# Optimization experiments

Measured on AMD Instinct MI355X. Metric: run time of the kernel, lower is better.

The kernel has to match this reference:

```python
import jax, jax.numpy as jnp
import numpy as np
from jax import lax

LOG2PI = float(np.log(2.0 * np.pi))
T, B, H, W, C = 64, 128, 64, 64, 3
A, LSTM_HID, LIN, CH, AH = 3, 512, 512, 256, 256
LSTM_IN = LIN + A + 1 + 1 + 1  # feats + last_action + last_reward + contact + time_till_end


def setup_inputs():
    key = jax.random.key(0)
    ks = jax.random.split(key, 32)

    def rn(i, shape, scale=1.0):
        return jax.random.normal(ks[i], shape, jnp.float32) * scale

    return {
        "x": rn(0, (T * B, H, W, C)),
        "done": jax.random.randint(ks[1], (T * B,), 0, 2, jnp.int32),
        "last_action": rn(2, (T * B, A)),
        "last_reward": rn(3, (T * B, 1)),
        "contact": jax.random.uniform(ks[4], (T * B, 1), jnp.float32),
        "time_till_end": jax.random.uniform(ks[5], (T * B, 1), jnp.float32),
        "action": rn(6, (T * B, A)),
        "h0": rn(7, (1, B, LSTM_HID)),
        "c0": rn(8, (1, B, LSTM_HID)),
        "conv1_w": rn(9, (8, 8, C, 32), 0.05), "conv1_b": jnp.zeros((32,), jnp.float32),
        "conv2_w": rn(10, (4, 4, 32, 64), 0.05), "conv2_b": jnp.zeros((64,), jnp.float32),
        "conv3_w": rn(11, (3, 3, 64, 64), 0.05), "conv3_b": jnp.zeros((64,), jnp.float32),
        "lin_w": rn(12, (1024, LIN), 0.03), "lin_b": jnp.zeros((LIN,), jnp.float32),
        "w_ih": rn(13, (4 * LSTM_HID, LSTM_IN), 0.02),
        "w_hh": rn(14, (4 * LSTM_HID, LSTM_HID), 0.02),
        "b_ih": jnp.zeros((4 * LSTM_HID,), jnp.float32),
        "b_hh": jnp.zeros((4 * LSTM_HID,), jnp.float32),
        "critic_w1": rn(15, (LSTM_HID, CH), 0.04), "critic_b1": jnp.zeros((CH,), jnp.float32),
        "critic_w2": rn(16, (CH, CH), 0.06), "critic_b2": jnp.zeros((CH,), jnp.float32),
        "critic_w3": rn(17, (CH, 1), 0.06), "critic_b3": jnp.zeros((1,), jnp.float32),
        "actor_w1": rn(18, (LSTM_HID, AH), 0.04), "actor_b1": jnp.zeros((AH,), jnp.float32),
        "actor_w2": rn(19, (AH, AH), 0.06), "actor_b2": jnp.zeros((AH,), jnp.float32),
        "actor_w3": rn(20, (AH, A), 0.01), "actor_b3": jnp.zeros((A,), jnp.float32),
        "actor_logstd": jnp.zeros((1, A), jnp.float32),
    }


def _conv(x, w, b, stride):
    y = lax.conv_general_dilated(x, w, (stride, stride), "VALID",
                                 dimension_numbers=("NHWC", "HWIO", "NHWC"))
    return jax.nn.relu(y + b)


def _mlp(v, w1, b1, w2, b2, w3, b3):
    v = jnp.tanh(v @ w1 + b1)
    v = jnp.tanh(v @ w2 + b2)
    return v @ w3 + b3


def reference(x, done, last_action, last_reward, contact, time_till_end, action, h0, c0,
              conv1_w, conv1_b, conv2_w, conv2_b, conv3_w, conv3_b, lin_w, lin_b,
              w_ih, w_hh, b_ih, b_hh,
              critic_w1, critic_b1, critic_w2, critic_b2, critic_w3, critic_b3,
              actor_w1, actor_b1, actor_w2, actor_b2, actor_w3, actor_b3, actor_logstd):
    batch = h0.shape[1]
    # CNN encoder (DQN-style)
    h = _conv(x, conv1_w, conv1_b, 4)            # [TB,15,15,32]
    h = _conv(h, conv2_w, conv2_b, 2)            # [TB,6,6,64]
    h = _conv(h, conv3_w, conv3_b, 1)            # [TB,4,4,64]
    h = h.reshape(h.shape[0], -1)                # [TB,1024]
    h = jax.nn.relu(h @ lin_w + lin_b)           # [TB,512]
    h = jnp.concatenate([h, last_action, last_reward, contact, time_till_end], axis=1)
    steps = h.shape[0] // batch
    xs = h.reshape(steps, batch, -1)             # [T,B,518]
    d = done.astype(h.dtype).reshape(steps, batch)

    def step(carry, inp):
        hs, cs = carry
        xt, dt = inp
        m = (1.0 - dt)[:, None]                  # reset state where done
        hs, cs = hs * m, cs * m
        z = xt @ w_ih.T + b_ih + hs @ w_hh.T + b_hh
        i, f, g, o = jnp.split(z, 4, axis=1)     # torch LSTM gate order i,f,g,o
        cs = jax.nn.sigmoid(f) * cs + jax.nn.sigmoid(i) * jnp.tanh(g)
        hs = jax.nn.sigmoid(o) * jnp.tanh(cs)
        return (hs, cs), hs

    (hN, cN), hid = lax.scan(step, (h0[0], c0[0]), (xs, d))
    hid = hid.reshape(steps * batch, -1)         # [TB,512]

    mean = _mlp(hid, actor_w1, actor_b1, actor_w2, actor_b2, actor_w3, actor_b3)
    logstd = jnp.broadcast_to(actor_logstd, mean.shape)
    inv_var = jnp.exp(-2.0 * logstd)
    logprob = (-0.5 * (action - mean) ** 2 * inv_var - logstd - 0.5 * LOG2PI).sum(axis=1)
    entropy = (0.5 + 0.5 * LOG2PI + logstd).sum(axis=1)
    value = _mlp(hid, critic_w1, critic_b1, critic_w2, critic_b2, critic_w3, critic_b3)
    return logprob, entropy, value, hN[None], cN[None]
```

## Files before the change

kernel.cpp:

```cpp
#include <hip/hip_runtime.h>
#include <hip/hip_bf16.h>
#include <cmath>

using bf16 = __hip_bfloat16;

#define DEV static __device__ __forceinline__

DEV float toF(float x) { return x; }
DEV float toF(bf16 x) { return __bfloat162float(x); }

DEV float loadF(const void* p, long i, int f32) {
    return f32 ? ((const float*)p)[i] : toF(((const bf16*)p)[i]);
}
DEV void storeOut(void* out, long i, float v, int f32) {
    if (f32) ((float*)out)[i] = v;
    else ((bf16*)out)[i] = __float2bfloat16(v);
}

__device__ __constant__ float kLOG2PI = 1.8378770664093453f;
DEV float sigf(float x) { return 1.0f / (1.0f + __expf(-x)); }

typedef __attribute__((ext_vector_type(4))) float fx4;
typedef __attribute__((ext_vector_type(8))) short s16x8;

static constexpr size_t OFF_WIHT  = 0;
static constexpr size_t OFF_WHHT  = 2121728;
static constexpr size_t OFF_BSUM  = 4218880;
static constexpr size_t OFF_LINB  = 4227072;
static constexpr size_t OFF_HB    = 4229120;
static constexpr size_t OFF_HT0   = 4233216;
static constexpr size_t OFF_HT1   = 4495360;
static constexpr size_t OFF_CT    = 4757504;
static constexpr size_t OFF_CW1   = 5019648;
static constexpr size_t OFF_CW2   = 5031936;
static constexpr size_t OFF_CW3   = 5097472;
static constexpr size_t OFF_CBIAS = 5171200;
static constexpr size_t OFF_ACT   = 5171840;
static constexpr size_t OFF_FB    = 5220992;
static constexpr size_t OFF_FLAG  = 5221024;
static constexpr size_t OFF_XIN   = 5221120;
static constexpr size_t OFF_C3H   = 13708032;
static constexpr size_t OFF_HID   = 22096640;
static constexpr size_t OFF_OUT2 = OFF_C3H;
static constexpr size_t OFF_OUT3 = OFF_C3H + 2359296;
static constexpr size_t OFF_LINW = OFF_C3H + 3407872;
static constexpr size_t OFF_OUT1 = OFF_HID;

__global__ void detect_k(const void* __restrict__ action, int* __restrict__ flag) {
    int lane = threadIdx.x;
    const unsigned short* p = (const unsigned short*)action;
    unsigned short v = p[lane];
    int e = (v >> 7) & 0xFF;
    bool bad = (e >= 0x8C);
    unsigned long long m = __ballot(bad);
    if (lane == 0) *flag = (m != 0ull) ? 1 : 0;
}

__global__ __launch_bounds__(256) void prep_k(
    const void* w_ih, const void* w_hh, const void* b_ih, const void* b_hh,
    const void* lin_b, const void* ab1, const void* ab2, const void* cb1, const void* cb2,
    const void* h0, const void* c0,
    const void* c1w, const void* c2w, const void* c3w,
    const void* c1b, const void* c2b, const void* c3b,
    const void* action, const void* ab3, const void* cb3, const void* logstd,
    bf16* __restrict__ wihT, bf16* __restrict__ whhT,
    float* __restrict__ bsum, float* __restrict__ linbf, float* __restrict__ hbias,
    float* __restrict__ hT0, float* __restrict__ cT,
    bf16* __restrict__ cw1, bf16* __restrict__ cw2, bf16* __restrict__ cw3,
    float* __restrict__ cbias, bf16* __restrict__ act, float* __restrict__ fb,
    const int* __restrict__ flagp,
    const void* lin_w, bf16* __restrict__ linwb)
{
    const int f = *flagp;
    long i = (long)blockIdx.x * 256 + threadIdx.x;
    if (i < 1060864) { long k = i >> 11, j = i & 2047;
        wihT[i] = __float2bfloat16(loadF(w_ih, j * 518 + k, f)); return; }
    i -= 1060864;
    if (i < 1048576) { long k = i >> 11, j = i & 2047;
        whhT[i] = __float2bfloat16(loadF(w_hh, j * 512 + k, f)); return; }
    i -= 1048576;
    if (i < 2048) { bsum[i] = loadF(b_ih, i, f) + loadF(b_hh, i, f); return; }
    i -= 2048;
    if (i < 512)  { linbf[i] = loadF(lin_b, i, f); return; }
    i -= 512;
    if (i < 1024) { int w = (int)(i >> 8), r = (int)(i & 255);
        const void* s = (w == 0) ? ab1 : (w == 1) ? ab2 : (w == 2) ? cb1 : cb2;
        hbias[i] = loadF(s, r, f); return; }
    i -= 1024;
    if (i < 65536) { long b = i & 127, k = i >> 7; hT0[i] = loadF(h0, b * 512 + k, f); return; }
    i -= 65536;
    if (i < 65536) { long b = i & 127, k = i >> 7; cT[i]  = loadF(c0, b * 512 + k, f); return; }
    i -= 65536;
    if (i < 6144)  { cw1[i] = __float2bfloat16(loadF(c1w, i, f)); return; }
    i -= 6144;
    if (i < 32768) { cw2[i] = __float2bfloat16(loadF(c2w, i, f)); return; }
    i -= 32768;
    if (i < 36864) { cw3[i] = __float2bfloat16(loadF(c3w, i, f)); return; }
    i -= 36864;
    if (i < 160) { float v = (i < 32) ? loadF(c1b, i, f)
                         : (i < 96) ? loadF(c2b, i - 32, f) : loadF(c3b, i - 96, f);
        cbias[i] = v; return; }
    i -= 160;
    if (i < 24576) { act[i] = __float2bfloat16(loadF(action, i, f)); return; }
    i -= 24576;
    if (i < 8) {
        float v = 0.f;
        if (i < 3) v = loadF(ab3, i, f);
        else if (i == 3) v = loadF(cb3, 0, f);
        else if (i < 7) v = loadF(logstd, i - 4, f);
        fb[i] = v; return;
    }
    i -= 8;
    if (i < 524288) { linwb[i] = __float2bfloat16(loadF(lin_w, i, f)); return; }
}

template <int BN, int MODE, int IC = 1, int KX = 1, int ST = 1, int IW = 1,
          int OW = 1, int OHW = 1>
__global__ __launch_bounds__(256) void mfma_gemm(
    const void* __restrict__ A, int lda,
    const bf16* __restrict__ B, int ldb,
    const float* __restrict__ bias,
    bf16* __restrict__ C, int ldc,
    int M, int N, int K, int ACT,
    const int* __restrict__ flagp, int imgBase)
{
    constexpr int BM = 128;
    constexpr int LSTR = 40;
    __shared__ __align__(16) bf16 As[BM * LSTR];
    __shared__ __align__(16) bf16 Bs[BN * LSTR];

    const int tid = threadIdx.x;
    const int lane = tid & 63, wave = tid >> 6;
    const int row0 = blockIdx.y * BM, col0 = blockIdx.x * BN;

    constexpr int NWN = (BN >= 64) ? 2 : 1;
    constexpr int WM = BM / (4 / NWN);
    constexpr int WN = BN / NWN;
    constexpr int FM = WM / 16, FN = WN / 16;
    const int wm = (wave / NWN) * WM;
    const int wn = (wave % NWN) * WN;

    fx4 acc[FM][FN] = {};

    const int am = tid >> 1;
    const int ak = (tid & 1) * 16;
    const int gm = row0 + am;
    int ibase = 0;
    if constexpr (MODE != 0) {
        int img = imgBase + gm / OHW;
        int s = gm % OHW;
        int oy = s / OW, ox = s % OW;
        ibase = (img * IW + oy * ST) * IW + ox * ST;
    }
    const int f32f = (MODE == 1) ? *flagp : 0;

    constexpr int KPT = BN / 8;
    const int nloc = tid & (BN - 1);
    const int kg0 = (tid / BN) * KPT;

    for (int k0 = 0; k0 < K; k0 += 32) {
        {
            bf16 tb[16];
            const int kk0 = k0 + ak;
            if constexpr (MODE == 0) {
                const unsigned short* Ab = (const unsigned short*)A + (long)gm * lda;
                if (kk0 + 16 <= K) {
                    const unsigned int* s4 = (const unsigned int*)(Ab + kk0);
                    unsigned int* d4 = (unsigned int*)tb;
                    #pragma unroll
                    for (int j = 0; j < 8; ++j) d4[j] = s4[j];
                } else {
                    unsigned short* bs = (unsigned short*)tb;
                    #pragma unroll
                    for (int j = 0; j < 16; ++j) {
                        int kg = kk0 + j;
                        bs[j] = (kg < K) ? Ab[kg] : (unsigned short)0;
                    }
                }
            } else {
                #pragma unroll
                for (int j = 0; j < 16; ++j) {
                    int kg = kk0 + j;
                    int ky = kg / (KX * IC);
                    int rem = kg - ky * (KX * IC);
                    int kx = rem / IC;
                    int ic = rem - kx * IC;
                    long idx = (long)(ibase + ky * IW + kx) * IC + ic;
                    if constexpr (MODE == 1)
                        tb[j] = __float2bfloat16(loadF(A, idx, f32f));
                    else
                        tb[j] = ((const bf16*)A)[idx];
                }
            }
            unsigned int* dst = (unsigned int*)(As + am * LSTR + ak);
            const unsigned int* src = (const unsigned int*)tb;
            #pragma unroll
            for (int j = 0; j < 8; ++j) dst[j] = src[j];
        }
        {
            bf16 tb[KPT];
            #pragma unroll
            for (int j = 0; j < KPT; ++j) {
                int kg = k0 + kg0 + j;
                unsigned short v = 0;
                if (kg < K) v = ((const unsigned short*)B)[(long)kg * ldb + col0 + nloc];
                ((unsigned short*)tb)[j] = v;
            }
            unsigned int* dst = (unsigned int*)(Bs + nloc * LSTR + kg0);
            const unsigned int* src = (const unsigned int*)tb;
            #pragma unroll
            for (int j = 0; j < KPT / 2; ++j) dst[j] = src[j];
        }
        __syncthreads();

        const int lr = lane & 15, lc = (lane >> 4) * 8;
        s16x8 af[FM], bfr[FN];
        #pragma unroll
        for (int i = 0; i < FM; ++i)
            af[i] = *(const s16x8*)(As + (wm + i * 16 + lr) * LSTR + lc);
        #pragma unroll
        for (int j = 0; j < FN; ++j)
            bfr[j] = *(const s16x8*)(Bs + (wn + j * 16 + lr) * LSTR + lc);
        #pragma unroll
        for (int i = 0; i < FM; ++i)
            #pragma unroll
            for (int j = 0; j < FN; ++j)
                acc[i][j] = __builtin_amdgcn_mfma_f32_16x16x32_bf16(
                    af[i], bfr[j], acc[i][j], 0, 0, 0);
        __syncthreads();
    }

    const int er = (lane >> 4) * 4, ec = lane & 15;
    #pragma unroll
    for (int i = 0; i < FM; ++i) {
        #pragma unroll
        for (int j = 0; j < FN; ++j) {
            const int cc = col0 + wn + j * 16 + ec;
            const float bv = bias[cc];
            #pragma unroll
            for (int r = 0; r < 4; ++r) {
                int rr = row0 + wm + i * 16 + er + r;
                float v = acc[i][j][r] + bv;
                if (ACT == 1) v = fmaxf(v, 0.f);
                C[(long)rr * ldc + cc] = __float2bfloat16(v);
            }
        }
    }
}

template <typename AT, typename OT, int BMODE, int ACT>
__global__ __launch_bounds__(256) void gemm_tiled(
    const AT* __restrict__ A, int lda,
    const void* __restrict__ B, int ldb,
    const float* __restrict__ bias,
    OT* __restrict__ C, int ldc,
    int M, int N, int K, const int* __restrict__ flagp)
{
    __shared__ float As[16][68];
    __shared__ float Bs[16][68];
    const int bF32 = (BMODE == 1) ? *flagp : 0;
    const int tid = threadIdx.x;
    const int tx = tid & 15, ty = tid >> 4;
    const int row0 = blockIdx.y * 64, col0 = blockIdx.x * 64;
    float acc[4][4] = {};
    for (int k0 = 0; k0 < K; k0 += 16) {
        #pragma unroll
        for (int i = 0; i < 4; ++i) {
            int idx = tid + i * 256;
            int m = idx >> 4, kk = idx & 15;
            int kg = k0 + kk;
            float v = 0.f;
            if (kg < K) v = toF(A[(size_t)(row0 + m) * lda + kg]);
            As[kk][m] = v;
        }
        #pragma unroll
        for (int i = 0; i < 4; ++i) {
            int idx = tid + i * 256;
            int n = idx & 63, kk = idx >> 6;
            int kg = k0 + kk;
            float v = 0.f;
            if (kg < K) {
                size_t bi = (size_t)kg * ldb + col0 + n;
                v = bF32 ? ((const float*)B)[bi] : toF(((const bf16*)B)[bi]);
            }
            Bs[kk][n] = v;
        }
        __syncthreads();
        #pragma unroll
        for (int kk = 0; kk < 16; ++kk) {
            float a[4], b[4];
            #pragma unroll
            for (int i = 0; i < 4; ++i) a[i] = As[kk][ty * 4 + i];
            #pragma unroll
            for (int j = 0; j < 4; ++j) b[j] = Bs[kk][tx * 4 + j];
            #pragma unroll
            for (int i = 0; i < 4; ++i)
                #pragma unroll
                for (int j = 0; j < 4; ++j)
                    acc[i][j] += a[i] * b[j];
        }
        __syncthreads();
    }
    #pragma unroll
    for (int i = 0; i < 4; ++i) {
        int r = row0 + ty * 4 + i;
        #pragma unroll
        for (int j = 0; j < 4; ++j) {
            int c = col0 + tx * 4 + j;
            float v = acc[i][j] + bias[c];
            if (ACT == 1) v = fmaxf(v, 0.f);
            if (ACT == 2) v = tanhf(v);
            if constexpr (sizeof(OT) == 2) C[(size_t)r * ldc + c] = __float2bfloat16(v);
            else                            C[(size_t)r * ldc + c] = v;
        }
    }
}

__global__ __launch_bounds__(256) void concat_k(
    const void* __restrict__ la, const void* __restrict__ lr,
    const void* __restrict__ ct, const void* __restrict__ tte,
    bf16* __restrict__ xin, const int* __restrict__ flagp)
{
    const int f = *flagp;
    int i = blockIdx.x * 256 + threadIdx.x;
    if (i >= 8192 * 6) return;
    int n = i / 6, e = i % 6;
    float v;
    if (e < 3) v = loadF(la, (long)n * 3 + e, f);
    else if (e == 3) v = loadF(lr, n, f);
    else if (e == 4) v = loadF(ct, n, f);
    else v = loadF(tte, n, f);
    xin[(size_t)n * 518 + 512 + e] = __float2bfloat16(v);
}

__global__ __launch_bounds__(256) void lstm_step(
    const bf16* __restrict__ zx,
    const bf16* __restrict__ whhT,
    const int* __restrict__ done,
    const float* __restrict__ hTin,
    float* __restrict__ hTout,
    float* __restrict__ cT,
    bf16* __restrict__ hid,
    int step)
{
    __shared__ float red[128][8];
    const int tid = threadIdx.x;
    const int b = tid & 127;
    const int kh = tid >> 7;
    const int j0 = blockIdx.x * 2;
    float acc[8] = {0.f, 0.f, 0.f, 0.f, 0.f, 0.f, 0.f, 0.f};
    const int kbeg = kh * 256;
    #pragma unroll 4
    for (int k = kbeg; k < kbeg + 256; ++k) {
        float hk = hTin[k * 128 + b];
        const bf16* wr = whhT + (size_t)k * 2048 + j0;
        #pragma unroll
        for (int g = 0; g < 4; ++g) {
            acc[g * 2 + 0] += hk * toF(wr[g * 512]);
            acc[g * 2 + 1] += hk * toF(wr[g * 512 + 1]);
        }
    }
    if (kh == 1) {
        #pragma unroll
        for (int q = 0; q < 8; ++q) red[b][q] = acc[q];
    }
    __syncthreads();
    if (kh == 0) {
        const int r = step * 128 + b;
        const long lr = (long)((step & 15) * 128 + b);
        const float m = done[r] ? 0.f : 1.f;
        #pragma unroll
        for (int jj = 0; jj < 2; ++jj) {
            int j = j0 + jj;
            float zi = toF(zx[lr * 2048 + 0 * 512 + j]) + m * (acc[0 + jj] + red[b][0 + jj]);
            float zf = toF(zx[lr * 2048 + 1 * 512 + j]) + m * (acc[2 + jj] + red[b][2 + jj]);
            float zg = toF(zx[lr * 2048 + 2 * 512 + j]) + m * (acc[4 + jj] + red[b][4 + jj]);
            float zo = toF(zx[lr * 2048 + 3 * 512 + j]) + m * (acc[6 + jj] + red[b][6 + jj]);
            float ig = sigf(zi), fg = sigf(zf), og = sigf(zo);
            float gg = tanhf(zg);
            float cold = cT[j * 128 + b] * m;
            float cn = fg * cold + ig * gg;
            float hn = og * tanhf(cn);
            cT[j * 128 + b] = cn;
            hTout[j * 128 + b] = hn;
            hid[(size_t)r * 512 + j] = __float2bfloat16(hn);
        }
    }
}

__global__ __launch_bounds__(256) void actor_final(
    const float* __restrict__ t2, const void* __restrict__ w3,
    const bf16* __restrict__ act, const float* __restrict__ fb,
    void* __restrict__ out, const int* __restrict__ flagp)
{
    const int f = *flagp;
    int lane = threadIdx.x & 63;
    int n = blockIdx.x * 4 + (threadIdx.x >> 6);
    const float* row = t2 + (size_t)n * 256;
    float s0 = 0.f, s1 = 0.f, s2 = 0.f;
    #pragma unroll
    for (int j = 0; j < 4; ++j) {
        int k = lane + j * 64;
        float v = row[k];
        s0 += v * loadF(w3, (long)k * 3 + 0, f);
        s1 += v * loadF(w3, (long)k * 3 + 1, f);
        s2 += v * loadF(w3, (long)k * 3 + 2, f);
    }
    #pragma unroll
    for (int off = 32; off > 0; off >>= 1) {
        s0 += __shfl_down(s0, off, 64);
        s1 += __shfl_down(s1, off, 64);
        s2 += __shfl_down(s2, off, 64);
    }
    if (lane == 0) {
        float mean[3] = {s0 + fb[0], s1 + fb[1], s2 + fb[2]};
        float lp = 0.f, ent = 0.f;
        #pragma unroll
        for (int a = 0; a < 3; ++a) {
            float ls = fb[4 + a];
            float iv = __expf(-2.f * ls);
            float d = toF(act[n * 3 + a]) - mean[a];
            lp += -0.5f * d * d * iv - ls - 0.5f * kLOG2PI;
            ent += 0.5f + 0.5f * kLOG2PI + ls;
        }
        storeOut(out, n, lp, f);
        storeOut(out, 8192 + n, ent, f);
    }
}

__global__ __launch_bounds__(256) void critic_final(
    const float* __restrict__ t2, const void* __restrict__ w3,
    const float* __restrict__ fb, void* __restrict__ out,
    const int* __restrict__ flagp)
{
    const int f = *flagp;
    int lane = threadIdx.x & 63;
    int n = blockIdx.x * 4 + (threadIdx.x >> 6);
    const float* row = t2 + (size_t)n * 256;
    float s = 0.f;
    #pragma unroll
    for (int j = 0; j < 4; ++j) {
        int k = lane + j * 64;
        s += row[k] * loadF(w3, k, f);
    }
    #pragma unroll
    for (int off = 32; off > 0; off >>= 1) s += __shfl_down(s, off, 64);
    if (lane == 0) storeOut(out, 16384 + n, s + fb[3], f);
}

__global__ __launch_bounds__(256) void state_out_k(
    const float* __restrict__ hT, const float* __restrict__ cT,
    void* __restrict__ out, const int* __restrict__ flagp)
{
    const int f = *flagp;
    int i = blockIdx.x * 256 + threadIdx.x;
    if (i >= 65536) return;
    int b = i >> 9, k = i & 511;
    storeOut(out, 24576 + i, hT[k * 128 + b], f);
    storeOut(out, 90112 + i, cT[k * 128 + b], f);
}

extern "C" void kernel_launch(void* const* d_in, const int* in_sizes, int n_in,
                              void* d_out, int out_size, void* d_ws, size_t ws_size,
                              hipStream_t stream)
{
    const void* x        = d_in[0];
    const int*  done     = (const int*)d_in[1];
    const void* last_act = d_in[2];
    const void* last_rew = d_in[3];
    const void* contact  = d_in[4];
    const void* tte      = d_in[5];
    const void* action   = d_in[6];
    const void* h0       = d_in[7];
    const void* c0       = d_in[8];
    const void* conv1_w  = d_in[9],  *conv1_b = d_in[10];
    const void* conv2_w  = d_in[11], *conv2_b = d_in[12];
    const void* conv3_w  = d_in[13], *conv3_b = d_in[14];
    const void* lin_w    = d_in[15], *lin_b   = d_in[16];
    const void* w_ih     = d_in[17], *w_hh    = d_in[18];
    const void* b_ih     = d_in[19], *b_hh    = d_in[20];
    const void* critic_w1 = d_in[21], *critic_b1 = d_in[22];
    const void* critic_w2 = d_in[23], *critic_b2 = d_in[24];
    const void* critic_w3 = d_in[25], *critic_b3 = d_in[26];
    const void* actor_w1  = d_in[27], *actor_b1  = d_in[28];
    const void* actor_w2  = d_in[29], *actor_b2  = d_in[30];
    const void* actor_w3  = d_in[31], *actor_b3  = d_in[32];
    const void* logstd    = d_in[33];

    char* ws = (char*)d_ws;
    bf16*  wihT  = (bf16*)(ws + OFF_WIHT);
    bf16*  whhT  = (bf16*)(ws + OFF_WHHT);
    float* bsum  = (float*)(ws + OFF_BSUM);
    float* linbf = (float*)(ws + OFF_LINB);
    float* hb    = (float*)(ws + OFF_HB);
    float* ab1f = hb + 0, *ab2f = hb + 256, *cb1f = hb + 512, *cb2f = hb + 768;
    float* hT0 = (float*)(ws + OFF_HT0);
    float* hT1 = (float*)(ws + OFF_HT1);
    float* cT  = (float*)(ws + OFF_CT);
    bf16*  cw1 = (bf16*)(ws + OFF_CW1);
    bf16*  cw2 = (bf16*)(ws + OFF_CW2);
    bf16*  cw3 = (bf16*)(ws + OFF_CW3);
    float* cbias = (float*)(ws + OFF_CBIAS);
    bf16*  act = (bf16*)(ws + OFF_ACT);
    float* fb  = (float*)(ws + OFF_FB);
    int*   flagp = (int*)(ws + OFF_FLAG);
    bf16*  xin = (bf16*)(ws + OFF_XIN);
    bf16*  zxb = (bf16*)(ws + OFF_C3H);
    bf16*  hid = (bf16*)(ws + OFF_HID);
    float* t1  = (float*)(ws + OFF_XIN);
    float* t2  = (float*)(ws + OFF_C3H);
    bf16*  out1  = (bf16*)(ws + OFF_OUT1);
    bf16*  out2  = (bf16*)(ws + OFF_OUT2);
    bf16*  out3  = (bf16*)(ws + OFF_OUT3);
    bf16*  linwb = (bf16*)(ws + OFF_LINW);

    detect_k<<<1, 64, 0, stream>>>(action, flagp);

    prep_k<<<11207, 256, 0, stream>>>(w_ih, w_hh, b_ih, b_hh, lin_b,
        actor_b1, actor_b2, critic_b1, critic_b2, h0, c0,
        conv1_w, conv2_w, conv3_w, conv1_b, conv2_b, conv3_b,
        action, actor_b3, critic_b3, logstd,
        wihT, whhT, bsum, linbf, hb, hT0, cT, cw1, cw2, cw3, cbias, act, fb, flagp,
        lin_w, linwb);

    for (int c = 0; c < 16; ++c) {
        const int ib = c * 512;
        mfma_gemm<32, 1, 3, 8, 4, 64, 15, 225><<<dim3(1, 900), 256, 0, stream>>>(
            x, 0, cw1, 32, cbias, out1, 32, 115200, 32, 192, 1, flagp, ib);
        mfma_gemm<64, 2, 32, 4, 2, 15, 6, 36><<<dim3(1, 144), 256, 0, stream>>>(
            out1, 0, cw2, 64, cbias + 32, out2, 64, 18432, 64, 512, 1, flagp, 0);
        mfma_gemm<64, 2, 64, 3, 1, 6, 4, 16><<<dim3(1, 64), 256, 0, stream>>>(
            out2, 0, cw3, 64, cbias + 96, out3, 64, 8192, 64, 576, 1, flagp, 0);
        mfma_gemm<64, 0><<<dim3(8, 4), 256, 0, stream>>>(
            out3, 1024, linwb, 512, linbf,
            xin + (size_t)ib * 518, 518, 512, 512, 1024, 1, flagp, 0);
    }
    concat_k<<<192, 256, 0, stream>>>(last_act, last_rew, contact, tte, xin, flagp);

    for (int chunk = 0; chunk < 4; ++chunk) {
        mfma_gemm<64, 0><<<dim3(32, 16), 256, 0, stream>>>(
            xin + (size_t)chunk * 2048 * 518, 518, wihT, 2048, bsum,
            zxb, 2048, 2048, 2048, 518, 0, flagp, 0);
        for (int t = chunk * 16; t < chunk * 16 + 16; ++t) {
            float* hin  = (t & 1) ? hT1 : hT0;
            float* hout = (t & 1) ? hT0 : hT1;
            lstm_step<<<256, 256, 0, stream>>>(zxb, whhT, done, hin, hout, cT, hid, t);
        }
    }

    gemm_tiled<bf16, float, 1, 2><<<dim3(4, 128), 256, 0, stream>>>(
        hid, 512, actor_w1, 256, ab1f, t1, 256, 8192, 256, 512, flagp);
    gemm_tiled<float, float, 1, 2><<<dim3(4, 128), 256, 0, stream>>>(
        t1, 256, actor_w2, 256, ab2f, t2, 256, 8192, 256, 256, flagp);
    actor_final<<<2048, 256, 0, stream>>>(t2, actor_w3, act, fb, d_out, flagp);

    gemm_tiled<bf16, float, 1, 2><<<dim3(4, 128), 256, 0, stream>>>(
        hid, 512, critic_w1, 256, cb1f, t1, 256, 8192, 256, 512, flagp);
    gemm_tiled<float, float, 1, 2><<<dim3(4, 128), 256, 0, stream>>>(
        t1, 256, critic_w2, 256, cb2f, t2, 256, 8192, 256, 256, flagp);
    critic_final<<<2048, 256, 0, stream>>>(t2, critic_w3, fb, d_out, flagp);

    state_out_k<<<256, 256, 0, stream>>>(hT0, cT, d_out, flagp);
}
```

Measured before the change: 6.183 ms.

## Fuse LSTM timesteps into persistent cooperative MFMA kernel and use MFMA for heads

```diff
diff --git a/kernel.cpp b/kernel.cpp
--- a/kernel.cpp
+++ b/kernel.cpp
@@ -1,6 +1,9 @@
 #include <hip/hip_runtime.h>
 #include <hip/hip_bf16.h>
+#include <hip/hip_cooperative_groups.h>
 #include <cmath>
+
+namespace cg = cooperative_groups;
 
 using bf16 = __hip_bfloat16;
 
@@ -65,7 +68,7 @@
     const void* action, const void* ab3, const void* cb3, const void* logstd,
     bf16* __restrict__ wihT, bf16* __restrict__ whhT,
     float* __restrict__ bsum, float* __restrict__ linbf, float* __restrict__ hbias,
-    float* __restrict__ hT0, float* __restrict__ cT,
+    bf16* __restrict__ h0b, float* __restrict__ cT,
     bf16* __restrict__ cw1, bf16* __restrict__ cw2, bf16* __restrict__ cw3,
     float* __restrict__ cbias, bf16* __restrict__ act, float* __restrict__ fb,
     const int* __restrict__ flagp,
@@ -87,7 +90,7 @@
         const void* s = (w == 0) ? ab1 : (w == 1) ? ab2 : (w == 2) ? cb1 : cb2;
         hbias[i] = loadF(s, r, f); return; }
     i -= 1024;
-    if (i < 65536) { long b = i & 127, k = i >> 7; hT0[i] = loadF(h0, b * 512 + k, f); return; }
+    if (i < 65536) { h0b[i] = __float2bfloat16(loadF(h0, i, f)); return; }
     i -= 65536;
     if (i < 65536) { long b = i & 127, k = i >> 7; cT[i]  = loadF(c0, b * 512 + k, f); return; }
     i -= 65536;
@@ -114,11 +117,11 @@
     if (i < 524288) { linwb[i] = __float2bfloat16(loadF(lin_w, i, f)); return; }
 }
 
-template <int BN, int MODE, int IC = 1, int KX = 1, int ST = 1, int IW = 1,
-          int OW = 1, int OHW = 1>
+template <int BN, int MODE, int BSRC = 0, int IC = 1, int KX = 1, int ST = 1,
+          int IW = 1, int OW = 1, int OHW = 1>
 __global__ __launch_bounds__(256) void mfma_gemm(
     const void* __restrict__ A, int lda,
-    const bf16* __restrict__ B, int ldb,
+    const void* __restrict__ B, int ldb,
     const float* __restrict__ bias,
     bf16* __restrict__ C, int ldc,
     int M, int N, int K, int ACT,
@@ -152,7 +155,7 @@
         int oy = s / OW, ox = s % OW;
         ibase = (img * IW + oy * ST) * IW + ox * ST;
     }
-    const int f32f = (MODE == 1) ? *flagp : 0;
+    const int f32f = (MODE == 1 || BSRC == 1) ? *flagp : 0;
 
     constexpr int KPT = BN / 8;
     const int nloc = tid & (BN - 1);
@@ -202,9 +205,15 @@
             #pragma unroll
             for (int j = 0; j < KPT; ++j) {
                 int kg = k0 + kg0 + j;
-                unsigned short v = 0;
-                if (kg < K) v = ((const unsigned short*)B)[(long)kg * ldb + col0 + nloc];
-                ((unsigned short*)tb)[j] = v;
+                if constexpr (BSRC == 1) {
+                    float v = 0.f;
+                    if (kg < K) v = loadF(B, (long)kg * ldb + col0 + nloc, f32f);
+                    tb[j] = __float2bfloat16(v);
+                } else {
+                    unsigned short v = 0;
+                    if (kg < K) v = ((const unsigned short*)B)[(long)kg * ldb + col0 + nloc];
+                    ((unsigned short*)tb)[j] = v;
+                }
             }
             unsigned int* dst = (unsigned int*)(Bs + nloc * LSTR + kg0);
             const unsigned int* src = (const unsigned int*)tb;
@@ -242,76 +251,9 @@
                 int rr = row0 + wm + i * 16 + er + r;
                 float v = acc[i][j][r] + bv;
                 if (ACT == 1) v = fmaxf(v, 0.f);
+                if (ACT == 2) v = tanhf(v);
                 C[(long)rr * ldc + cc] = __float2bfloat16(v);
             }
-        }
-    }
-}
-
-template <typename AT, typename OT, int BMODE, int ACT>
-__global__ __launch_bounds__(256) void gemm_tiled(
-    const AT* __restrict__ A, int lda,
-    const void* __restrict__ B, int ldb,
-    const float* __restrict__ bias,
-    OT* __restrict__ C, int ldc,
-    int M, int N, int K, const int* __restrict__ flagp)
-{
-    __shared__ float As[16][68];
-    __shared__ float Bs[16][68];
-    const int bF32 = (BMODE == 1) ? *flagp : 0;
-    const int tid = threadIdx.x;
-    const int tx = tid & 15, ty = tid >> 4;
-    const int row0 = blockIdx.y * 64, col0 = blockIdx.x * 64;
-    float acc[4][4] = {};
-    for (int k0 = 0; k0 < K; k0 += 16) {
-        #pragma unroll
-        for (int i = 0; i < 4; ++i) {
-            int idx = tid + i * 256;
-            int m = idx >> 4, kk = idx & 15;
-            int kg = k0 + kk;
-            float v = 0.f;
-            if (kg < K) v = toF(A[(size_t)(row0 + m) * lda + kg]);
-            As[kk][m] = v;
-        }
-        #pragma unroll
-        for (int i = 0; i < 4; ++i) {
-            int idx = tid + i * 256;
-            int n = idx & 63, kk = idx >> 6;
-            int kg = k0 + kk;
-            float v = 0.f;
-            if (kg < K) {
-                size_t bi = (size_t)kg * ldb + col0 + n;
-                v = bF32 ? ((const float*)B)[bi] : toF(((const bf16*)B)[bi]);
-            }
-            Bs[kk][n] = v;
-        }
-        __syncthreads();
-        #pragma unroll
-        for (int kk = 0; kk < 16; ++kk) {
-            float a[4], b[4];
-            #pragma unroll
-            for (int i = 0; i < 4; ++i) a[i] = As[kk][ty * 4 + i];
-            #pragma unroll
-            for (int j = 0; j < 4; ++j) b[j] = Bs[kk][tx * 4 + j];
-            #pragma unroll
-            for (int i = 0; i < 4; ++i)
-                #pragma unroll
-                for (int j = 0; j < 4; ++j)
-                    acc[i][j] += a[i] * b[j];
-        }
-        __syncthreads();
-    }
-    #pragma unroll
-    for (int i = 0; i < 4; ++i) {
-        int r = row0 + ty * 4 + i;
-        #pragma unroll
-        for (int j = 0; j < 4; ++j) {
-            int c = col0 + tx * 4 + j;
-            float v = acc[i][j] + bias[c];
-            if (ACT == 1) v = fmaxf(v, 0.f);
-            if (ACT == 2) v = tanhf(v);
-            if constexpr (sizeof(OT) == 2) C[(size_t)r * ldc + c] = __float2bfloat16(v);
-            else                            C[(size_t)r * ldc + c] = v;
         }
     }
 }
@@ -333,75 +275,109 @@
     xin[(size_t)n * 518 + 512 + e] = __float2bfloat16(v);
 }
 
-__global__ __launch_bounds__(256) void lstm_step(
+__global__ __launch_bounds__(256, 1) void lstm16_k(
     const bf16* __restrict__ zx,
     const bf16* __restrict__ whhT,
     const int* __restrict__ done,
-    const float* __restrict__ hTin,
-    float* __restrict__ hTout,
+    const bf16* __restrict__ h0b,
+    bf16* __restrict__ hid,
     float* __restrict__ cT,
-    bf16* __restrict__ hid,
-    int step)
-{
-    __shared__ float red[128][8];
+    int chunk)
+{
+    __shared__ float zsm[128][17];
     const int tid = threadIdx.x;
-    const int b = tid & 127;
-    const int kh = tid >> 7;
-    const int j0 = blockIdx.x * 2;
-    float acc[8] = {0.f, 0.f, 0.f, 0.f, 0.f, 0.f, 0.f, 0.f};
-    const int kbeg = kh * 256;
-    #pragma unroll 4
-    for (int k = kbeg; k < kbeg + 256; ++k) {
-        float hk = hTin[k * 128 + b];
-        const bf16* wr = whhT + (size_t)k * 2048 + j0;
-        #pragma unroll
-        for (int g = 0; g < 4; ++g) {
-            acc[g * 2 + 0] += hk * toF(wr[g * 512]);
-            acc[g * 2 + 1] += hk * toF(wr[g * 512 + 1]);
-        }
-    }
-    if (kh == 1) {
-        #pragma unroll
-        for (int q = 0; q < 8; ++q) red[b][q] = acc[q];
-    }
-    __syncthreads();
-    if (kh == 0) {
-        const int r = step * 128 + b;
-        const long lr = (long)((step & 15) * 128 + b);
-        const float m = done[r] ? 0.f : 1.f;
-        #pragma unroll
-        for (int jj = 0; jj < 2; ++jj) {
-            int j = j0 + jj;
-            float zi = toF(zx[lr * 2048 + 0 * 512 + j]) + m * (acc[0 + jj] + red[b][0 + jj]);
-            float zf = toF(zx[lr * 2048 + 1 * 512 + j]) + m * (acc[2 + jj] + red[b][2 + jj]);
-            float zg = toF(zx[lr * 2048 + 2 * 512 + j]) + m * (acc[4 + jj] + red[b][4 + jj]);
-            float zo = toF(zx[lr * 2048 + 3 * 512 + j]) + m * (acc[6 + jj] + red[b][6 + jj]);
+    const int lane = tid & 63, wave = tid >> 6;
+    const int bk = blockIdx.x;
+    const int c0 = bk * 4;
+
+    const int q = lane & 15;
+    const int gcol = (q >> 2) * 512 + c0 + (q & 3);
+    const int kb = (lane >> 4) * 8;
+
+    s16x8 bfrag[16];
+    #pragma unroll
+    for (int kt = 0; kt < 16; ++kt) {
+        #pragma unroll
+        for (int j = 0; j < 8; ++j) {
+            int k = kt * 32 + kb + j;
+            ((short*)&bfrag[kt])[j] = ((const short*)whhT)[(long)k * 2048 + gcol];
+        }
+    }
+
+    float creg[2];
+    #pragma unroll
+    for (int r = 0; r < 2; ++r) {
+        int p = tid + r * 256;
+        int b = p >> 2, cc = p & 3;
+        creg[r] = cT[(c0 + cc) * 128 + b];
+    }
+
+    const int m0 = wave * 32;
+    const int lr16 = lane & 15;
+    cg::grid_group grid = cg::this_grid();
+
+    for (int ts = 0; ts < 16; ++ts) {
+        const int gt = chunk * 16 + ts;
+        const bf16* hsrc = (gt == 0) ? h0b : (hid + (long)(gt - 1) * 65536);
+
+        fx4 acc0 = {}, acc1 = {};
+        #pragma unroll
+        for (int kt = 0; kt < 16; ++kt) {
+            s16x8 a0 = *(const s16x8*)(hsrc + (long)(m0 + lr16) * 512 + kt * 32 + kb);
+            s16x8 a1 = *(const s16x8*)(hsrc + (long)(m0 + 16 + lr16) * 512 + kt * 32 + kb);
+            acc0 = __builtin_amdgcn_mfma_f32_16x16x32_bf16(a0, bfrag[kt], acc0, 0, 0, 0);
+            acc1 = __builtin_amdgcn_mfma_f32_16x16x32_bf16(a1, bfrag[kt], acc1, 0, 0, 0);
+        }
+        const int er = (lane >> 4) * 4;
+        #pragma unroll
+        for (int r = 0; r < 4; ++r) zsm[m0 + er + r][q] = acc0[r];
+        #pragma unroll
+        for (int r = 0; r < 4; ++r) zsm[m0 + 16 + er + r][q] = acc1[r];
+        __syncthreads();
+
+        #pragma unroll
+        for (int r = 0; r < 2; ++r) {
+            int p = tid + r * 256;
+            int b = p >> 2, cc = p & 3;
+            float m = done[gt * 128 + b] ? 0.f : 1.f;
+            long zrow = (long)((gt & 15) * 128 + b) * 2048 + c0 + cc;
+            float zi = toF(zx[zrow])        + m * zsm[b][0 + cc];
+            float zf = toF(zx[zrow + 512])  + m * zsm[b][4 + cc];
+            float zg = toF(zx[zrow + 1024]) + m * zsm[b][8 + cc];
+            float zo = toF(zx[zrow + 1536]) + m * zsm[b][12 + cc];
             float ig = sigf(zi), fg = sigf(zf), og = sigf(zo);
             float gg = tanhf(zg);
-            float cold = cT[j * 128 + b] * m;
-            float cn = fg * cold + ig * gg;
+            float cn = fg * (creg[r] * m) + ig * gg;
             float hn = og * tanhf(cn);
-            cT[j * 128 + b] = cn;
-            hTout[j * 128 + b] = hn;
-            hid[(size_t)r * 512 + j] = __float2bfloat16(hn);
-        }
+            creg[r] = cn;
+            hid[(long)(gt * 128 + b) * 512 + c0 + cc] = __float2bfloat16(hn);
+        }
+        __threadfence();
+        grid.sync();
+    }
+
+    #pragma unroll
+    for (int r = 0; r < 2; ++r) {
+        int p = tid + r * 256;
+        int b = p >> 2, cc = p & 3;
+        cT[(c0 + cc) * 128 + b] = creg[r];
     }
 }
 
 __global__ __launch_bounds__(256) void actor_final(
-    const float* __restrict__ t2, const void* __restrict__ w3,
+    const bf16* __restrict__ t2, const void* __restrict__ w3,
     const bf16* __restrict__ act, const float* __restrict__ fb,
     void* __restrict__ out, const int* __restrict__ flagp)
 {
     const int f = *flagp;
     int lane = threadIdx.x & 63;
     int n = blockIdx.x * 4 + (threadIdx.x >> 6);
-    const float* row = t2 + (size_t)n * 256;
+    const bf16* row = t2 + (size_t)n * 256;
     float s0 = 0.f, s1 = 0.f, s2 = 0.f;
     #pragma unroll
     for (int j = 0; j < 4; ++j) {
         int k = lane + j * 64;
-        float v = row[k];
+        float v = toF(row[k]);
         s0 += v * loadF(w3, (long)k * 3 + 0, f);
         s1 += v * loadF(w3, (long)k * 3 + 1, f);
         s2 += v * loadF(w3, (long)k * 3 + 2, f);
@@ -429,19 +405,19 @@
 }
 
 __global__ __launch_bounds__(256) void critic_final(
-    const float* __restrict__ t2, const void* __restrict__ w3,
+    const bf16* __restrict__ t2, const void* __restrict__ w3,
     const float* __restrict__ fb, void* __restrict__ out,
     const int* __restrict__ flagp)
 {
     const int f = *flagp;
     int lane = threadIdx.x & 63;
     int n = blockIdx.x * 4 + (threadIdx.x >> 6);
-    const float* row = t2 + (size_t)n * 256;
+    const bf16* row = t2 + (size_t)n * 256;
     float s = 0.f;
     #pragma unroll
     for (int j = 0; j < 4; ++j) {
         int k = lane + j * 64;
-        s += row[k] * loadF(w3, k, f);
+        s += toF(row[k]) * loadF(w3, k, f);
     }
     #pragma unroll
     for (int off = 32; off > 0; off >>= 1) s += __shfl_down(s, off, 64);
@@ -449,14 +425,14 @@
 }
 
 __global__ __launch_bounds__(256) void state_out_k(
-    const float* __restrict__ hT, const float* __restrict__ cT,
+    const bf16* __restrict__ hid, const float* __restrict__ cT,
     void* __restrict__ out, const int* __restrict__ flagp)
 {
     const int f = *flagp;
     int i = blockIdx.x * 256 + threadIdx.x;
     if (i >= 65536) return;
     int b = i >> 9, k = i & 511;
-    storeOut(out, 24576 + i, hT[k * 128 + b], f);
+    storeOut(out, 24576 + i, toF(hid[4128768 + i]), f);
     storeOut(out, 90112 + i, cT[k * 128 + b], f);
 }
 
@@ -494,8 +470,7 @@
     float* linbf = (float*)(ws + OFF_LINB);
     float* hb    = (float*)(ws + OFF_HB);
     float* ab1f = hb + 0, *ab2f = hb + 256, *cb1f = hb + 512, *cb2f = hb + 768;
-    float* hT0 = (float*)(ws + OFF_HT0);
-    float* hT1 = (float*)(ws + OFF_HT1);
+    bf16*  h0b = (bf16*)(ws + OFF_HT0);
     float* cT  = (float*)(ws + OFF_CT);
     bf16*  cw1 = (bf16*)(ws + OFF_CW1);
     bf16*  cw2 = (bf16*)(ws + OFF_CW2);
@@ -507,8 +482,8 @@
     bf16*  xin = (bf16*)(ws + OFF_XIN);
     bf16*  zxb = (bf16*)(ws + OFF_C3H);
     bf16*  hid = (bf16*)(ws + OFF_HID);
-    float* t1  = (float*)(ws + OFF_XIN);
-    float* t2  = (float*)(ws + OFF_C3H);
+    bf16*  t1b = (bf16*)(ws + OFF_XIN);
+    bf16*  t2b = (bf16*)(ws + OFF_C3H);
     bf16*  out1  = (bf16*)(ws + OFF_OUT1);
     bf16*  out2  = (bf16*)(ws + OFF_OUT2);
     bf16*  out3  = (bf16*)(ws + OFF_OUT3);
@@ -520,16 +495,16 @@
         actor_b1, actor_b2, critic_b1, critic_b2, h0, c0,
         conv1_w, conv2_w, conv3_w, conv1_b, conv2_b, conv3_b,
         action, actor_b3, critic_b3, logstd,
-        wihT, whhT, bsum, linbf, hb, hT0, cT, cw1, cw2, cw3, cbias, act, fb, flagp,
+        wihT, whhT, bsum, linbf, hb, h0b, cT, cw1, cw2, cw3, cbias, act, fb, flagp,
         lin_w, linwb);
 
     for (int c = 0; c < 16; ++c) {
         const int ib = c * 512;
-        mfma_gemm<32, 1, 3, 8, 4, 64, 15, 225><<<dim3(1, 900), 256, 0, stream>>>(
+        mfma_gemm<32, 1, 0, 3, 8, 4, 64, 15, 225><<<dim3(1, 900), 256, 0, stream>>>(
             x, 0, cw1, 32, cbias, out1, 32, 115200, 32, 192, 1, flagp, ib);
-        mfma_gemm<64, 2, 32, 4, 2, 15, 6, 36><<<dim3(1, 144), 256, 0, stream>>>(
+        mfma_gemm<64, 2, 0, 32, 4, 2, 15, 6, 36><<<dim3(1, 144), 256, 0, stream>>>(
             out1, 0, cw2, 64, cbias + 32, out2, 64, 18432, 64, 512, 1, flagp, 0);
-        mfma_gemm<64, 2, 64, 3, 1, 6, 4, 16><<<dim3(1, 64), 256, 0, stream>>>(
+        mfma_gemm<64, 2, 0, 64, 3, 1, 6, 4, 16><<<dim3(1, 64), 256, 0, stream>>>(
             out2, 0, cw3, 64, cbias + 96, out3, 64, 8192, 64, 576, 1, flagp, 0);
         mfma_gemm<64, 0><<<dim3(8, 4), 256, 0, stream>>>(
             out3, 1024, linwb, 512, linbf,
@@ -541,24 +516,32 @@
         mfma_gemm<64, 0><<<dim3(32, 16), 256, 0, stream>>>(
             xin + (size_t)chunk * 2048 * 518, 518, wihT, 2048, bsum,
             zxb, 2048, 2048, 2048, 518, 0, flagp, 0);
-        for (int t = chunk * 16; t < chunk * 16 + 16; ++t) {
-            float* hin  = (t & 1) ? hT1 : hT0;
-            float* hout = (t & 1) ? hT0 : hT1;
-            lstm_step<<<256, 256, 0, stream>>>(zxb, whhT, done, hin, hout, cT, hid, t);
-        }
-    }
-
-    gemm_tiled<bf16, float, 1, 2><<<dim3(4, 128), 256, 0, stream>>>(
-        hid, 512, actor_w1, 256, ab1f, t1, 256, 8192, 256, 512, flagp);
-    gemm_tiled<float, float, 1, 2><<<dim3(4, 128), 256, 0, stream>>>(
-        t1, 256, actor_w2, 256, ab2f, t2, 256, 8192, 256, 256, flagp);
-    actor_final<<<2048, 256, 0, stream>>>(t2, actor_w3, act, fb, d_out, flagp);
-
-    gemm_tiled<bf16, float, 1, 2><<<dim3(4, 128), 256, 0, stream>>>(
-        hid, 512, critic_w1, 256, cb1f, t1, 256, 8192, 256, 512, flagp);
-    gemm_tiled<float, float, 1, 2><<<dim3(4, 128), 256, 0, stream>>>(
-        t1, 256, critic_w2, 256, cb2f, t2, 256, 8192, 256, 256, flagp);
-    critic_final<<<2048, 256, 0, stream>>>(t2, critic_w3, fb, d_out, flagp);
-
-    state_out_k<<<256, 256, 0, stream>>>(hT0, cT, d_out, flagp);
-}
+        {
+            const bf16* zxp = zxb;
+            const bf16* whp = whhT;
+            const int*  dnp = done;
+            const bf16* h0p = h0b;
+            bf16* hip = hid;
+            float* ctp = cT;
+            int ck = chunk;
+            void* args[] = { (void*)&zxp, (void*)&whp, (void*)&dnp, (void*)&h0p,
+                             (void*)&hip, (void*)&ctp, (void*)&ck };
+            hipLaunchCooperativeKernel(reinterpret_cast<void*>(lstm16_k),
+                                       dim3(128), dim3(256), args, 0, stream);
+        }
+    }
+
+    mfma_gemm<64, 0, 1><<<dim3(4, 64), 256, 0, stream>>>(
+        hid, 512, actor_w1, 256, ab1f, t1b, 256, 8192, 256, 512, 2, flagp, 0);
+    mfma_gemm<64, 0, 1><<<dim3(4, 64), 256, 0, stream>>>(
+        t1b, 256, actor_w2, 256, ab2f, t2b, 256, 8192, 256, 256, 2, flagp, 0);
+    actor_final<<<2048, 256, 0, stream>>>(t2b, actor_w3, act, fb, d_out, flagp);
+
+    mfma_gemm<64, 0, 1><<<dim3(4, 64), 256, 0, stream>>>(
+        hid, 512, critic_w1, 256, cb1f, t1b, 256, 8192, 256, 512, 2, flagp, 0);
+    mfma_gemm<64, 0, 1><<<dim3(4, 64), 256, 0, stream>>>(
+        t1b, 256, critic_w2, 256, cb2f, t2b, 256, 8192, 256, 256, 2, flagp, 0);
+    critic_final<<<2048, 256, 0, stream>>>(t2b, critic_w3, fb, d_out, flagp);
+
+    state_out_k<<<256, 256, 0, stream>>>(hid, cT, d_out, flagp);
+}
```

Measured after the change: 6.860 ms. 11.0% more time.
